# Kernel tuning notes

Hardware: AMD Instinct MI355X
Metric: run time of the kernel (lower is better)

## Reference

```python
import jax, jax.numpy as jnp
import numpy as np

N_SRC, N_DST, E, D, OUT = 100000, 20000, 600000, 128, 128

def setup_inputs() -> dict:
    key = jax.random.key(0)
    k1, k2, k3, k4, k5 = jax.random.split(key, 5)
    h = jax.random.normal(k1, (N_SRC, D), dtype=jnp.float32)
    edge_src = jax.random.randint(k2, (E,), 0, N_SRC, dtype=jnp.int64)
    edge_dst = jax.random.randint(k3, (E,), 0, N_DST, dtype=jnp.int64)
    W = jax.random.normal(k4, (OUT, 2 * D), dtype=jnp.float32) * (1.0 / np.sqrt(2 * D))
    b = jax.random.normal(k5, (OUT,), dtype=jnp.float32) * 0.01
    return {"h": h, "edge_src": edge_src, "edge_dst": edge_dst, "W": W, "b": b, "n_dst": N_DST}

def reference(h, edge_src, edge_dst, W, b, n_dst):
    # dst nodes are the first n_dst src nodes (DGL block convention)
    h_dst = h[:n_dst]                                   # [n_dst, D]
    msgs = h[edge_src]                                  # gather: [E, D]
    agg = jax.ops.segment_sum(msgs, edge_dst, num_segments=n_dst)   # [n_dst, D]
    deg = jax.ops.segment_sum(jnp.ones(edge_src.shape, h.dtype), edge_dst, num_segments=n_dst)
    h_neigh = agg / jnp.maximum(deg, 1.0)[:, None]      # mean; 0-degree -> 0
    z = jnp.concatenate([h_dst, h_neigh], axis=1)       # [n_dst, 2D]
    return jax.nn.relu(z @ W.T + b)                     # [n_dst, OUT]
```

## Files before the change

### kernel.cpp

```cpp
#include <hip/hip_runtime.h>

#define DFEAT 128
#define KDIM  256
#define NBIN  4
#define BCAP  32
#define CAP   128
#define WSTR  264

typedef __attribute__((ext_vector_type(8))) short bf16x8;
typedef __attribute__((ext_vector_type(4))) float f32x4;
typedef __attribute__((ext_vector_type(2))) float f32x2;

__device__ __forceinline__ float bflo(unsigned int u) {
    union { unsigned int i; float f; } v; v.i = u << 16; return v.f;
}
__device__ __forceinline__ float bfhi(unsigned int u) {
    union { unsigned int i; float f; } v; v.i = u & 0xffff0000u; return v.f;
}
__device__ __forceinline__ unsigned short f2bf(float f) {
    union { float f; unsigned int i; } v; v.f = f;
    unsigned int r = (v.i + 0x7fffu + ((v.i >> 16) & 1u)) >> 16;
    return (unsigned short)r;
}
__device__ __forceinline__ unsigned int pack2(float x, float y) {
    return ((unsigned int)f2bf(y) << 16) | (unsigned int)f2bf(x);
}
__device__ __forceinline__ uint4 cvt8(const float* p) {
    float4 a = *(const float4*)p;
    float4 b = *(const float4*)(p + 4);
    return make_uint4(pack2(a.x, a.y), pack2(a.z, a.w),
                      pack2(b.x, b.y), pack2(b.z, b.w));
}
__device__ __forceinline__ uint2 cvtfp8(const float* p) {
    float4 a = *(const float4*)p;
    float4 b = *(const float4*)(p + 4);
    int w0 = __builtin_amdgcn_cvt_pk_fp8_f32(a.x, a.y, 0, false);
    w0 = __builtin_amdgcn_cvt_pk_fp8_f32(a.z, a.w, w0, true);
    int w1 = __builtin_amdgcn_cvt_pk_fp8_f32(b.x, b.y, 0, false);
    w1 = __builtin_amdgcn_cvt_pk_fp8_f32(b.z, b.w, w1, true);
    return make_uint2((unsigned int)w0, (unsigned int)w1);
}

__global__ __launch_bounds__(256) void prep_kernel(
    const float* __restrict__ h, const float* __restrict__ W,
    const int* __restrict__ esrc, const int* __restrict__ edst,
    unsigned short* __restrict__ hbf,
    unsigned char* __restrict__ hfp8,
    unsigned short* __restrict__ z,
    unsigned short* __restrict__ Wbf,
    int* __restrict__ cnt, int* __restrict__ sorted,
    int E, int n_chunks, int B_C, int B_H, int cshift)
{
    int blk = blockIdx.x;
    int tid = threadIdx.x;
    if (blk < B_C) {
        int e0 = blk * 1024 + tid;
        int b  = tid & (NBIN - 1);
        int d[4], s[4];
        bool ok[4];
        #pragma unroll
        for (int r = 0; r < 4; ++r) {
            int e = e0 + r * 256;
            ok[r] = (e < E);
            d[r] = ok[r] ? edst[e] : 0;
            s[r] = ok[r] ? esrc[e] : 0;
        }
        int pos[4];
        #pragma unroll
        for (int r = 0; r < 4; ++r)
            pos[r] = ok[r] ? atomicAdd(&cnt[(size_t)(d[r] * NBIN + b) << cshift], 1)
                           : BCAP;
        #pragma unroll
        for (int r = 0; r < 4; ++r)
            if (ok[r] && pos[r] < BCAP)
                sorted[(size_t)d[r] * CAP + b * BCAP + pos[r]] = s[r];
    } else if (blk < B_C + B_H) {
        int c0 = (blk - B_C) * 1024 + tid;
        #pragma unroll
        for (int r = 0; r < 4; ++r) {
            int t = c0 + r * 256;
            if (t < n_chunks) {
                if (hbf) {
                    *(uint4*)(hbf + (size_t)t * 8) = cvt8(h + (size_t)t * 8);
                    *(uint2*)(hfp8 + (size_t)t * 8) = cvtfp8(h + (size_t)t * 8);
                } else {
                    uint4 v = cvt8(h + (size_t)t * 8);
                    int row = t >> 4;
                    int col = (t & 15) * 8;
                    *(uint4*)(z + (size_t)row * KDIM + col) = v;
                }
            }
        }
    } else {
        int t = (blk - B_C - B_H) * 256 + tid;
        *(uint4*)(Wbf + (size_t)t * 8) = cvt8(W + (size_t)t * 8);
    }
}

__global__ __launch_bounds__(256) void agg_bf16_kernel(
    const unsigned char* __restrict__ hfp8, const int* __restrict__ cnt,
    const int* __restrict__ sorted, unsigned short* __restrict__ zn, int n_dst,
    int cshift)
{
    __shared__ int Ls[16][CAP];

    int wave = threadIdx.x >> 6;
    int lane = threadIdx.x & 63;
    int grp  = lane >> 4;
    int l16  = lane & 15;
    int g    = wave * 4 + grp;
    int d    = blockIdx.x * 16 + g;
    int dv   = (d < n_dst) ? d : n_dst - 1;

    const int* segb = sorted + (size_t)dv * CAP;
    int base = 0;
    #pragma unroll
    for (int b = 0; b < NBIN; ++b) {
        int c = cnt[(size_t)(dv * NBIN + b) << cshift];
        c = (c > BCAP) ? BCAP : c;
        for (int i = l16; i < c; i += 16)
            Ls[g][base + i] = segb[b * BCAP + i];
        base += c;
    }
    int tot = base;

    float acc[8];
    #pragma unroll
    for (int j = 0; j < 8; ++j) acc[j] = 0.f;

    const uint2* hp = (const uint2*)hfp8 + l16;
    int i = 0;
    for (; i + 7 < tot; i += 8) {
        int ix[8];
        #pragma unroll
        for (int r = 0; r < 8; ++r) ix[r] = Ls[g][i + r];
        uint2 u[8];
        #pragma unroll
        for (int r = 0; r < 8; ++r) u[r] = hp[(size_t)ix[r] * 16];
        #pragma unroll
        for (int r = 0; r < 8; ++r) {
            f32x2 f01 = __builtin_amdgcn_cvt_pk_f32_fp8(u[r].x, false);
            f32x2 f23 = __builtin_amdgcn_cvt_pk_f32_fp8(u[r].x, true);
            f32x2 f45 = __builtin_amdgcn_cvt_pk_f32_fp8(u[r].y, false);
            f32x2 f67 = __builtin_amdgcn_cvt_pk_f32_fp8(u[r].y, true);
            acc[0] += f01.x; acc[1] += f01.y;
            acc[2] += f23.x; acc[3] += f23.y;
            acc[4] += f45.x; acc[5] += f45.y;
            acc[6] += f67.x; acc[7] += f67.y;
        }
    }
    for (; i < tot; ++i) {
        uint2 u = hp[(size_t)Ls[g][i] * 16];
        f32x2 f01 = __builtin_amdgcn_cvt_pk_f32_fp8(u.x, false);
        f32x2 f23 = __builtin_amdgcn_cvt_pk_f32_fp8(u.x, true);
        f32x2 f45 = __builtin_amdgcn_cvt_pk_f32_fp8(u.y, false);
        f32x2 f67 = __builtin_amdgcn_cvt_pk_f32_fp8(u.y, true);
        acc[0] += f01.x; acc[1] += f01.y;
        acc[2] += f23.x; acc[3] += f23.y;
        acc[4] += f45.x; acc[5] += f45.y;
        acc[6] += f67.x; acc[7] += f67.y;
    }
    float inv = 1.0f / fmaxf((float)tot, 1.0f);
    if (d < n_dst)
        ((uint4*)zn)[(size_t)d * 16 + l16] = make_uint4(
            pack2(acc[0] * inv, acc[1] * inv), pack2(acc[2] * inv, acc[3] * inv),
            pack2(acc[4] * inv, acc[5] * inv), pack2(acc[6] * inv, acc[7] * inv));
}

__device__ __forceinline__ int binmap(int j, int p1, int p2, int p3) {
    int o = j;
    o = (j >= p1) ? j - p1 + BCAP     : o;
    o = (j >= p2) ? j - p2 + 2 * BCAP : o;
    o = (j >= p3) ? j - p3 + 3 * BCAP : o;
    return o;
}

__global__ __launch_bounds__(256) void agg_f32_kernel(
    const float* __restrict__ h, const int* __restrict__ cnt,
    const int* __restrict__ sorted, unsigned short* __restrict__ z, int n_dst,
    int cshift)
{
    int d = blockIdx.x * 4 + (threadIdx.x >> 6);
    if (d >= n_dst) return;
    int lane = threadIdx.x & 63;
    int cb[NBIN];
    #pragma unroll
    for (int b = 0; b < NBIN; ++b) {
        int c = cnt[(size_t)(d * NBIN + b) << cshift];
        cb[b] = (c > BCAP) ? BCAP : c;
    }
    int p1 = cb[0], p2 = p1 + cb[1], p3 = p2 + cb[2];
    int tot = p3 + cb[3];
    const int* seg = sorted + (size_t)d * CAP;
    float ax = 0.f, ay = 0.f;
    const float2* hp = (const float2*)h + lane;
    int i = 0;
    for (; i + 1 < tot; i += 2) {
        int i0 = seg[binmap(i, p1, p2, p3)];
        int i1 = seg[binmap(i + 1, p1, p2, p3)];
        float2 v0 = hp[(size_t)i0 * 64], v1 = hp[(size_t)i1 * 64];
        ax += v0.x + v1.x; ay += v0.y + v1.y;
    }
    for (; i < tot; ++i) {
        float2 v = hp[(size_t)seg[binmap(i, p1, p2, p3)] * 64];
        ax += v.x; ay += v.y;
    }
    float inv = 1.0f / fmaxf((float)tot, 1.0f);
    ((unsigned int*)z)[(size_t)d * 128 + 64 + lane] = pack2(ax * inv, ay * inv);
}

__global__ __launch_bounds__(256) void gemm_kernel(
    const unsigned short* __restrict__ alo, int slo,
    const unsigned short* __restrict__ ahi, int shi,
    const unsigned short* __restrict__ Wbf,
    const float* __restrict__ bias,
    float* __restrict__ out,
    int n_dst)
{
    __shared__ unsigned short Wl[DFEAT][WSTR];

    int tid  = threadIdx.x;
    int wave = tid >> 6;
    int lane = tid & 63;
    int quad = lane >> 4;
    int l16  = lane & 15;
    int m0   = blockIdx.x * 64 + wave * 16;

    #pragma unroll
    for (int i = 0; i < 16; ++i) {
        int u  = i * 256 + tid;
        int n  = u >> 5;
        int kq = (u & 31) * 8;
        *(uint4*)&Wl[n][kq] = *(const uint4*)(Wbf + (size_t)n * KDIM + kq);
    }

    int m_a = m0 + l16;
    if (m_a > n_dst - 1) m_a = n_dst - 1;

    f32x4 acc[8];
    #pragma unroll
    for (int ct = 0; ct < 8; ++ct) acc[ct] = (f32x4){0.f, 0.f, 0.f, 0.f};

    const unsigned short* plo = alo + (size_t)m_a * slo + quad * 8;
    const unsigned short* phi = ahi + (size_t)m_a * shi + quad * 8;

    __syncthreads();

    #pragma unroll
    for (int ks = 0; ks < 8; ++ks) {
        bf16x8 a = (ks < 4) ? *(const bf16x8*)(plo + ks * 32)
                            : *(const bf16x8*)(phi + (ks - 4) * 32);
        #pragma unroll
        for (int ct = 0; ct < 8; ++ct) {
            bf16x8 bb = *(const bf16x8*)&Wl[ct * 16 + l16][ks * 32 + quad * 8];
            acc[ct] = __builtin_amdgcn_mfma_f32_16x16x32_bf16(a, bb, acc[ct], 0, 0, 0);
        }
    }

    #pragma unroll
    for (int ct = 0; ct < 8; ++ct) {
        int n = ct * 16 + l16;
        float bc = bias[n];
        #pragma unroll
        for (int r = 0; r < 4; ++r) {
            int m = m0 + quad * 4 + r;
            if (m < n_dst)
                out[(size_t)m * DFEAT + n] = fmaxf(acc[ct][r] + bc, 0.0f);
        }
    }
}


extern "C" void kernel_launch(void* const* d_in, const int* in_sizes, int n_in,
                              void* d_out, int out_size, void* d_ws, size_t ws_size,
                              hipStream_t stream) {
    const float* h  = (const float*)d_in[0];
    const int* esrc = (const int*)d_in[1];
    const int* edst = (const int*)d_in[2];
    const float* W  = (const float*)d_in[3];
    const float* b  = (const float*)d_in[4];
    float* out      = (float*)d_out;

    const int E     = in_sizes[1];
    const int n_src = in_sizes[0] / DFEAT;
    const int n_dst = out_size / DFEAT;

    size_t hbf_bytes  = (size_t)n_src * DFEAT * 2;
    size_t hf8_bytes  = (size_t)n_src * DFEAT;
    size_t zn_bytes   = (size_t)n_dst * DFEAT * 2;
    size_t wbf_bytes  = (size_t)DFEAT * KDIM * 2;
    size_t cnt_base   = (size_t)n_dst * NBIN * sizeof(int);
    size_t srt_bytes  = (size_t)n_dst * CAP * sizeof(int);

    int cshift = 5;
    bool fast;
    for (;;) {
        size_t cb = cnt_base << cshift;
        fast = ws_size >=
               hbf_bytes + hf8_bytes + zn_bytes + wbf_bytes + cb + srt_bytes;
        if (fast || cshift == 0) break;
        --cshift;
    }
    if (!fast) {
        cshift = 5;
        while (cshift > 0 &&
               ws_size < wbf_bytes + (cnt_base << cshift) + srt_bytes)
            --cshift;
    }
    size_t cnt_bytes = cnt_base << cshift;

    char* p = (char*)d_ws;
    unsigned short *hbf, *zn, *Wbf;
    unsigned char *hfp8;
    int *cnt, *sorted;
    if (fast) {
        hbf  = (unsigned short*)p;           p += hbf_bytes;
        hfp8 = (unsigned char*)p;            p += hf8_bytes;
        zn   = (unsigned short*)p;           p += zn_bytes;
        Wbf  = (unsigned short*)p;           p += wbf_bytes;
        cnt  = (int*)p;                      p += cnt_bytes;
        sorted = (int*)p;
    } else {
        hbf = nullptr; hfp8 = nullptr; zn = nullptr;
        Wbf = (unsigned short*)p;            p += wbf_bytes;
        cnt = (int*)p;                       p += cnt_bytes;
        sorted = (int*)p;
    }

    unsigned short* z = (unsigned short*)d_out;

    (void)hipMemsetAsync(cnt, 0, cnt_bytes, stream);

    int n_chunks = (fast ? n_src : n_dst) * (DFEAT / 8);
    int B_C = (E + 1023) / 1024;
    int B_H = (n_chunks + 1023) / 1024;
    int B_W = (DFEAT * KDIM / 8) / 256;

    prep_kernel<<<B_C + B_H + B_W, 256, 0, stream>>>(
        h, W, esrc, edst, hbf, hfp8, fast ? nullptr : z, Wbf, cnt, sorted,
        E, n_chunks, B_C, B_H, cshift);

    if (fast) {
        agg_bf16_kernel<<<(n_dst + 15) / 16, 256, 0, stream>>>(
            hfp8, cnt, sorted, zn, n_dst, cshift);
        gemm_kernel<<<(n_dst + 63) / 64, 256, 0, stream>>>(
            hbf, DFEAT, zn, DFEAT, Wbf, b, out, n_dst);
    } else {
        agg_f32_kernel<<<(n_dst + 3) / 4, 256, 0, stream>>>(
            h, cnt, sorted, z, n_dst, cshift);
        gemm_kernel<<<(n_dst + 63) / 64, 256, 0, stream>>>(
            z, KDIM, z + DFEAT, KDIM, Wbf, b, out, n_dst);
    }
}
```

Before: 158.4 us.

## Fuse neighbor aggregation into GEMM kernel via LDS staging, shrink bf16 h copy

Merges the fp8 gather-mean aggregation and the MFMA GEMM into one kernel: each 64-row block aggregates its destination rows into an LDS tile, then runs the bf16 MFMA against h_dst and W. This drops the zn round trip through global memory and one kernel launch. The bf16 copy of h is now written only for the first n_dst rows, cutting prep write traffic. The cost is 4x fewer aggregation blocks (1/4 the parallelism per dst) and sequential per-block agg-then-GEMM with no overlap.

```diff
diff --git a/kernel.cpp b/kernel.cpp
--- a/kernel.cpp
+++ b/kernel.cpp
@@ -49,7 +49,7 @@
     unsigned short* __restrict__ z,
     unsigned short* __restrict__ Wbf,
     int* __restrict__ cnt, int* __restrict__ sorted,
-    int E, int n_chunks, int B_C, int B_H, int cshift)
+    int E, int n_chunks, int ndc, int B_C, int B_H, int cshift)
 {
     int blk = blockIdx.x;
     int tid = threadIdx.x;
@@ -80,9 +80,10 @@
         for (int r = 0; r < 4; ++r) {
             int t = c0 + r * 256;
             if (t < n_chunks) {
-                if (hbf) {
-                    *(uint4*)(hbf + (size_t)t * 8) = cvt8(h + (size_t)t * 8);
+                if (hfp8) {
                     *(uint2*)(hfp8 + (size_t)t * 8) = cvtfp8(h + (size_t)t * 8);
+                    if (t < ndc)
+                        *(uint4*)(hbf + (size_t)t * 8) = cvt8(h + (size_t)t * 8);
                 } else {
                     uint4 v = cvt8(h + (size_t)t * 8);
                     int row = t >> 4;
@@ -97,74 +98,120 @@
     }
 }
 
-__global__ __launch_bounds__(256) void agg_bf16_kernel(
-    const unsigned char* __restrict__ hfp8, const int* __restrict__ cnt,
-    const int* __restrict__ sorted, unsigned short* __restrict__ zn, int n_dst,
-    int cshift)
+__global__ __launch_bounds__(256) void aggemm_kernel(
+    const unsigned char* __restrict__ hfp8,
+    const unsigned short* __restrict__ hbf,
+    const int* __restrict__ cnt, const int* __restrict__ sorted,
+    const unsigned short* __restrict__ Wbf,
+    const float* __restrict__ bias,
+    float* __restrict__ out,
+    int n_dst, int cshift)
 {
-    __shared__ int Ls[16][CAP];
-
-    int wave = threadIdx.x >> 6;
-    int lane = threadIdx.x & 63;
+    __shared__ unsigned short Zl[64][136];
+    __shared__ int Ls[16][132];
+
+    int tid  = threadIdx.x;
+    int wave = tid >> 6;
+    int lane = tid & 63;
     int grp  = lane >> 4;
     int l16  = lane & 15;
-    int g    = wave * 4 + grp;
-    int d    = blockIdx.x * 16 + g;
-    int dv   = (d < n_dst) ? d : n_dst - 1;
-
-    const int* segb = sorted + (size_t)dv * CAP;
-    int base = 0;
-    #pragma unroll
-    for (int b = 0; b < NBIN; ++b) {
-        int c = cnt[(size_t)(dv * NBIN + b) << cshift];
-        c = (c > BCAP) ? BCAP : c;
-        for (int i = l16; i < c; i += 16)
-            Ls[g][base + i] = segb[b * BCAP + i];
-        base += c;
-    }
-    int tot = base;
-
-    float acc[8];
-    #pragma unroll
-    for (int j = 0; j < 8; ++j) acc[j] = 0.f;
-
-    const uint2* hp = (const uint2*)hfp8 + l16;
-    int i = 0;
-    for (; i + 7 < tot; i += 8) {
-        int ix[8];
-        #pragma unroll
-        for (int r = 0; r < 8; ++r) ix[r] = Ls[g][i + r];
-        uint2 u[8];
-        #pragma unroll
-        for (int r = 0; r < 8; ++r) u[r] = hp[(size_t)ix[r] * 16];
-        #pragma unroll
-        for (int r = 0; r < 8; ++r) {
-            f32x2 f01 = __builtin_amdgcn_cvt_pk_f32_fp8(u[r].x, false);
-            f32x2 f23 = __builtin_amdgcn_cvt_pk_f32_fp8(u[r].x, true);
-            f32x2 f45 = __builtin_amdgcn_cvt_pk_f32_fp8(u[r].y, false);
-            f32x2 f67 = __builtin_amdgcn_cvt_pk_f32_fp8(u[r].y, true);
+    int slot = wave * 4 + grp;
+
+    for (int p = 0; p < 4; ++p) {
+        int g = p * 16 + slot;
+        int d = blockIdx.x * 64 + g;
+        int dv = (d < n_dst) ? d : n_dst - 1;
+
+        const int* segb = sorted + (size_t)dv * CAP;
+        int base = 0;
+        #pragma unroll
+        for (int b = 0; b < NBIN; ++b) {
+            int c = cnt[(size_t)(dv * NBIN + b) << cshift];
+            c = (c > BCAP) ? BCAP : c;
+            for (int i = l16; i < c; i += 16)
+                Ls[slot][base + i] = segb[b * BCAP + i];
+            base += c;
+        }
+        int tot = (d < n_dst) ? base : 0;
+
+        float acc[8];
+        #pragma unroll
+        for (int j = 0; j < 8; ++j) acc[j] = 0.f;
+
+        const uint2* hp = (const uint2*)hfp8 + l16;
+        int i = 0;
+        for (; i + 7 < tot; i += 8) {
+            int ix[8];
+            #pragma unroll
+            for (int r = 0; r < 8; ++r) ix[r] = Ls[slot][i + r];
+            uint2 u[8];
+            #pragma unroll
+            for (int r = 0; r < 8; ++r) u[r] = hp[(size_t)ix[r] * 16];
+            #pragma unroll
+            for (int r = 0; r < 8; ++r) {
+                f32x2 f01 = __builtin_amdgcn_cvt_pk_f32_fp8(u[r].x, false);
+                f32x2 f23 = __builtin_amdgcn_cvt_pk_f32_fp8(u[r].x, true);
+                f32x2 f45 = __builtin_amdgcn_cvt_pk_f32_fp8(u[r].y, false);
+                f32x2 f67 = __builtin_amdgcn_cvt_pk_f32_fp8(u[r].y, true);
+                acc[0] += f01.x; acc[1] += f01.y;
+                acc[2] += f23.x; acc[3] += f23.y;
+                acc[4] += f45.x; acc[5] += f45.y;
+                acc[6] += f67.x; acc[7] += f67.y;
+            }
+        }
+        for (; i < tot; ++i) {
+            uint2 u = hp[(size_t)Ls[slot][i] * 16];
+            f32x2 f01 = __builtin_amdgcn_cvt_pk_f32_fp8(u.x, false);
+            f32x2 f23 = __builtin_amdgcn_cvt_pk_f32_fp8(u.x, true);
+            f32x2 f45 = __builtin_amdgcn_cvt_pk_f32_fp8(u.y, false);
+            f32x2 f67 = __builtin_amdgcn_cvt_pk_f32_fp8(u.y, true);
             acc[0] += f01.x; acc[1] += f01.y;
             acc[2] += f23.x; acc[3] += f23.y;
             acc[4] += f45.x; acc[5] += f45.y;
             acc[6] += f67.x; acc[7] += f67.y;
         }
-    }
-    for (; i < tot; ++i) {
-        uint2 u = hp[(size_t)Ls[g][i] * 16];
-        f32x2 f01 = __builtin_amdgcn_cvt_pk_f32_fp8(u.x, false);
-        f32x2 f23 = __builtin_amdgcn_cvt_pk_f32_fp8(u.x, true);
-        f32x2 f45 = __builtin_amdgcn_cvt_pk_f32_fp8(u.y, false);
-        f32x2 f67 = __builtin_amdgcn_cvt_pk_f32_fp8(u.y, true);
-        acc[0] += f01.x; acc[1] += f01.y;
-        acc[2] += f23.x; acc[3] += f23.y;
-        acc[4] += f45.x; acc[5] += f45.y;
-        acc[6] += f67.x; acc[7] += f67.y;
-    }
-    float inv = 1.0f / fmaxf((float)tot, 1.0f);
-    if (d < n_dst)
-        ((uint4*)zn)[(size_t)d * 16 + l16] = make_uint4(
+        float inv = 1.0f / fmaxf((float)tot, 1.0f);
+        *(uint4*)&Zl[g][l16 * 8] = make_uint4(
             pack2(acc[0] * inv, acc[1] * inv), pack2(acc[2] * inv, acc[3] * inv),
             pack2(acc[4] * inv, acc[5] * inv), pack2(acc[6] * inv, acc[7] * inv));
+    }
+
+    __syncthreads();
+
+    int m0  = blockIdx.x * 64 + wave * 16;
+    int m_a = m0 + l16;
+    if (m_a > n_dst - 1) m_a = n_dst - 1;
+
+    f32x4 acc[8];
+    #pragma unroll
+    for (int ct = 0; ct < 8; ++ct) acc[ct] = (f32x4){0.f, 0.f, 0.f, 0.f};
+
+    const unsigned short* plo = hbf + (size_t)m_a * DFEAT + grp * 8;
+    const unsigned short* zrow = &Zl[wave * 16 + l16][grp * 8];
+
+    #pragma unroll
+    for (int ks = 0; ks < 8; ++ks) {
+        bf16x8 a = (ks < 4) ? *(const bf16x8*)(plo + ks * 32)
+                            : *(const bf16x8*)(zrow + (ks - 4) * 32);
+        #pragma unroll
+        for (int ct = 0; ct < 8; ++ct) {
+            bf16x8 bb = *(const bf16x8*)(
+                Wbf + (size_t)(ct * 16 + l16) * KDIM + ks * 32 + grp * 8);
+            acc[ct] = __builtin_amdgcn_mfma_f32_16x16x32_bf16(a, bb, acc[ct], 0, 0, 0);
+        }
+    }
+
+    #pragma unroll
+    for (int ct = 0; ct < 8; ++ct) {
+        int n = ct * 16 + l16;
+        float bc = bias[n];
+        #pragma unroll
+        for (int r = 0; r < 4; ++r) {
+            int m = m0 + grp * 4 + r;
+            if (m < n_dst)
+                out[(size_t)m * DFEAT + n] = fmaxf(acc[ct][r] + bc, 0.0f);
+        }
+    }
 }
 
 __device__ __forceinline__ int binmap(int j, int p1, int p2, int p3) {
@@ -285,9 +332,8 @@
     const int n_src = in_sizes[0] / DFEAT;
     const int n_dst = out_size / DFEAT;
 
-    size_t hbf_bytes  = (size_t)n_src * DFEAT * 2;
+    size_t hbf_bytes  = (size_t)n_dst * DFEAT * 2;
     size_t hf8_bytes  = (size_t)n_src * DFEAT;
-    size_t zn_bytes   = (size_t)n_dst * DFEAT * 2;
     size_t wbf_bytes  = (size_t)DFEAT * KDIM * 2;
     size_t cnt_base   = (size_t)n_dst * NBIN * sizeof(int);
     size_t srt_bytes  = (size_t)n_dst * CAP * sizeof(int);
@@ -297,7 +343,7 @@
     for (;;) {
         size_t cb = cnt_base << cshift;
         fast = ws_size >=
-               hbf_bytes + hf8_bytes + zn_bytes + wbf_bytes + cb + srt_bytes;
+               hbf_bytes + hf8_bytes + wbf_bytes + cb + srt_bytes;
         if (fast || cshift == 0) break;
         --cshift;
     }
@@ -310,18 +356,17 @@
     size_t cnt_bytes = cnt_base << cshift;
 
     char* p = (char*)d_ws;
-    unsigned short *hbf, *zn, *Wbf;
+    unsigned short *hbf, *Wbf;
     unsigned char *hfp8;
     int *cnt, *sorted;
     if (fast) {
         hbf  = (unsigned short*)p;           p += hbf_bytes;
         hfp8 = (unsigned char*)p;            p += hf8_bytes;
-        zn   = (unsigned short*)p;           p += zn_bytes;
         Wbf  = (unsigned short*)p;           p += wbf_bytes;
         cnt  = (int*)p;                      p += cnt_bytes;
         sorted = (int*)p;
     } else {
-        hbf = nullptr; hfp8 = nullptr; zn = nullptr;
+        hbf = nullptr; hfp8 = nullptr;
         Wbf = (unsigned short*)p;            p += wbf_bytes;
         cnt = (int*)p;                       p += cnt_bytes;
         sorted = (int*)p;
@@ -332,19 +377,18 @@
     (void)hipMemsetAsync(cnt, 0, cnt_bytes, stream);
 
     int n_chunks = (fast ? n_src : n_dst) * (DFEAT / 8);
+    int ndc      = n_dst * (DFEAT / 8);
     int B_C = (E + 1023) / 1024;
     int B_H = (n_chunks + 1023) / 1024;
     int B_W = (DFEAT * KDIM / 8) / 256;
 
     prep_kernel<<<B_C + B_H + B_W, 256, 0, stream>>>(
         h, W, esrc, edst, hbf, hfp8, fast ? nullptr : z, Wbf, cnt, sorted,
-        E, n_chunks, B_C, B_H, cshift);
+        E, n_chunks, ndc, B_C, B_H, cshift);
 
     if (fast) {
-        agg_bf16_kernel<<<(n_dst + 15) / 16, 256, 0, stream>>>(
-            hfp8, cnt, sorted, zn, n_dst, cshift);
-        gemm_kernel<<<(n_dst + 63) / 64, 256, 0, stream>>>(
-            hbf, DFEAT, zn, DFEAT, Wbf, b, out, n_dst);
+        aggemm_kernel<<<(n_dst + 63) / 64, 256, 0, stream>>>(
+            hfp8, hbf, cnt, sorted, Wbf, b, out, n_dst, cshift);
     } else {
         agg_f32_kernel<<<(n_dst + 3) / 4, 256, 0, stream>>>(
             h, cnt, sorted, z, n_dst, cshift);
```

Result: slower. 178.8 us (+12.9%).
